# Kernel tuning notes

Measured on AMD Instinct MI355X. Metric: run time of the kernel, lower is better.

The kernel has to match this reference:

```python
import jax, jax.numpy as jnp
import numpy as np

N, B, D_IN, D_MID, D_OUT = 2048, 64, 768, 512, 128


def setup_inputs() -> dict:
    key = jax.random.key(0)
    ks = jax.random.split(key, 6)
    x = jax.random.normal(ks[0], (N, B, D_IN), dtype=jnp.float32)
    W1 = jax.random.normal(ks[1], (D_IN, D_MID), dtype=jnp.float32) * 0.02
    b1 = jax.random.normal(ks[2], (D_MID,), dtype=jnp.float32) * 0.02
    W2 = jax.random.normal(ks[3], (D_MID, D_OUT), dtype=jnp.float32) * 0.02
    b2 = jax.random.normal(ks[4], (D_OUT,), dtype=jnp.float32) * 0.02
    # per-sample segment lengths in [1, N//2] so segments are non-empty and in-range
    batch_list = jax.random.randint(ks[5], (B,), 1, N // 2, dtype=jnp.int32)
    return {"x": x, "W1": W1, "b1": b1, "W2": W2, "b2": b2,
            "batch_list": batch_list, "batch_size": B}


def reference(x, W1, b1, W2, b2, batch_list, batch_size):
    # x.reshape(-1, batch_size, 768).transpose(0, 1) -> (B, N, 768)
    xb = x.reshape(-1, batch_size, D_IN).transpose(1, 0, 2)
    h = jax.nn.relu(jnp.einsum('bnd,dm->bnm', xb, W1) + b1)
    x0 = jnp.einsum('bnm,mo->bno', h, W2) + b2  # (B, N, D_OUT)

    n = x0.shape[1]
    # torch code: batch_list.insert(0, 0); segment i = rows [L[i], L[i]+L[i+1]) of x_0[i]
    # i.e. start_i = (0 if i == 0 else batch_list[i-1]), len_i = batch_list[i]
    starts = jnp.concatenate([jnp.zeros((1,), jnp.int32), batch_list[:-1]])
    lens = batch_list
    j = jnp.arange(n, dtype=jnp.int32)  # (N,)
    mask = (j[None, :] >= starts[:, None]) & (j[None, :] < (starts + lens)[:, None])  # (B, N)
    neg = jnp.asarray(-jnp.inf, x0.dtype)
    x1 = jnp.where(mask[:, :, None], x0, neg).max(axis=1)  # (B, D_OUT)
    x1_probs = jnp.argmax(jax.nn.softmax(x1, axis=-1), axis=-1)
    return (x1, x1_probs)
```

## Files before the change

### kernel.cpp

```cpp
#include <hip/hip_runtime.h>
#include <math.h>

#define N_TOK 2048
#define BATCH 64
#define DIN   768
#define DMID  512
#define DOUT  128
#define TILE_N 64
#define KC    64
#define MC    128

__device__ __forceinline__ void atomicMaxFloat(float* addr, float val) {
    if (val >= 0.0f) atomicMax((int*)addr, __float_as_int(val));
    else             atomicMin((unsigned int*)addr, __float_as_uint(val));
}

__global__ void init_kernel(float* __restrict__ x1) {
    int i = blockIdx.x * blockDim.x + threadIdx.x;
    if (i < BATCH * DOUT) x1[i] = -INFINITY;
}

__global__ __launch_bounds__(256, 3) void fused_kernel(
    const float* __restrict__ x,
    const float* __restrict__ W1,
    const float* __restrict__ b1,
    const float* __restrict__ W2,
    const float* __restrict__ b2,
    const int*   __restrict__ batch_list,
    float* __restrict__ x1)
{
    const int b    = blockIdx.y;
    const int row0 = blockIdx.x * TILE_N;

    const int start = (b == 0) ? 0 : batch_list[b - 1];
    const int len   = batch_list[b];
    const int end   = start + len;
    if (row0 >= end || row0 + TILE_N <= start) return;

    __shared__ float xs[TILE_N][KC];
    __shared__ float hs[TILE_N][MC];

    const int tid = threadIdx.x;
    const int tr  = tid >> 5;
    const int tc  = tid & 31;

    float acc2[8][4];
    #pragma unroll
    for (int r = 0; r < 8; ++r)
        #pragma unroll
        for (int c = 0; c < 4; ++c) acc2[r][c] = 0.0f;

    for (int mc = 0; mc < DMID; mc += MC) {
        float acc1[8][4];
        #pragma unroll
        for (int r = 0; r < 8; ++r)
            #pragma unroll
            for (int c = 0; c < 4; ++c) acc1[r][c] = 0.0f;

        const float* W1c = W1 + mc + tc * 4;

        for (int kc = 0; kc < DIN; kc += KC) {
            __syncthreads();
            #pragma unroll
            for (int j = 0; j < 4; ++j) {
                const int i  = tid + j * 256;
                const int r  = i >> 4;
                const int kq = i & 15;
                *(float4*)&xs[r][kq * 4] =
                    *(const float4*)&x[((size_t)(row0 + r) * BATCH + b) * DIN + kc + kq * 4];
            }
            __syncthreads();

            #pragma unroll 4
            for (int k = 0; k < KC; ++k) {
                const float4 w = *(const float4*)&W1c[(size_t)(kc + k) * DMID];
                float xv[8];
                #pragma unroll
                for (int r = 0; r < 8; ++r) xv[r] = xs[tr * 8 + r][k];
                #pragma unroll
                for (int r = 0; r < 8; ++r) {
                    acc1[r][0] = fmaf(xv[r], w.x, acc1[r][0]);
                    acc1[r][1] = fmaf(xv[r], w.y, acc1[r][1]);
                    acc1[r][2] = fmaf(xv[r], w.z, acc1[r][2]);
                    acc1[r][3] = fmaf(xv[r], w.w, acc1[r][3]);
                }
            }
        }

        {
            const float4 bb = *(const float4*)&b1[mc + tc * 4];
            const float bv[4] = {bb.x, bb.y, bb.z, bb.w};
            #pragma unroll
            for (int r = 0; r < 8; ++r) {
                float4 hv;
                hv.x = fmaxf(acc1[r][0] + bv[0], 0.0f);
                hv.y = fmaxf(acc1[r][1] + bv[1], 0.0f);
                hv.z = fmaxf(acc1[r][2] + bv[2], 0.0f);
                hv.w = fmaxf(acc1[r][3] + bv[3], 0.0f);
                *(float4*)&hs[tr * 8 + r][tc * 4] = hv;
            }
        }
        __syncthreads();

        const float* W2c = W2 + (size_t)mc * DOUT + tc * 4;
        #pragma unroll 4
        for (int kk = 0; kk < MC; ++kk) {
            const float4 w = *(const float4*)&W2c[(size_t)kk * DOUT];
            float hv[8];
            #pragma unroll
            for (int r = 0; r < 8; ++r) hv[r] = hs[tr * 8 + r][kk];
            #pragma unroll
            for (int r = 0; r < 8; ++r) {
                acc2[r][0] = fmaf(hv[r], w.x, acc2[r][0]);
                acc2[r][1] = fmaf(hv[r], w.y, acc2[r][1]);
                acc2[r][2] = fmaf(hv[r], w.z, acc2[r][2]);
                acc2[r][3] = fmaf(hv[r], w.w, acc2[r][3]);
            }
        }
    }

    const float4 bb2 = *(const float4*)&b2[tc * 4];
    const float bv2[4] = {bb2.x, bb2.y, bb2.z, bb2.w};
    float cmax[4] = {-INFINITY, -INFINITY, -INFINITY, -INFINITY};
    #pragma unroll
    for (int r = 0; r < 8; ++r) {
        const int row = row0 + tr * 8 + r;
        const bool in = (row >= start) && (row < end);
        #pragma unroll
        for (int c = 0; c < 4; ++c) {
            const float v = acc2[r][c] + bv2[c];
            if (in) cmax[c] = fmaxf(cmax[c], v);
        }
    }

    float (*red)[DOUT] = (float(*)[DOUT])xs;
    #pragma unroll
    for (int c = 0; c < 4; ++c) red[tr][tc * 4 + c] = cmax[c];
    __syncthreads();

    if (tid < DOUT) {
        float m = red[0][tid];
        #pragma unroll
        for (int r = 1; r < 8; ++r) m = fmaxf(m, red[r][tid]);
        atomicMaxFloat(&x1[b * DOUT + tid], m);
    }
}

__global__ void argmax_kernel(const float* __restrict__ x1, float* __restrict__ probs) {
    int b = blockIdx.x * blockDim.x + threadIdx.x;
    if (b >= BATCH) return;
    const float* row = x1 + b * DOUT;
    float best = row[0];
    int bi = 0;
    for (int c = 1; c < DOUT; ++c) {
        float v = row[c];
        if (v > best) { best = v; bi = c; }
    }
    probs[b] = (float)bi;
}

extern "C" void kernel_launch(void* const* d_in, const int* in_sizes, int n_in,
                              void* d_out, int out_size, void* d_ws, size_t ws_size,
                              hipStream_t stream) {
    const float* x          = (const float*)d_in[0];
    const float* W1         = (const float*)d_in[1];
    const float* b1         = (const float*)d_in[2];
    const float* W2         = (const float*)d_in[3];
    const float* b2         = (const float*)d_in[4];
    const int*   batch_list = (const int*)d_in[5];

    float* x1    = (float*)d_out;
    float* probs = x1 + BATCH * DOUT;

    init_kernel<<<(BATCH * DOUT + 255) / 256, 256, 0, stream>>>(x1);

    dim3 grid(N_TOK / TILE_N, BATCH);
    fused_kernel<<<grid, 256, 0, stream>>>(x, W1, b1, W2, b2, batch_list, x1);

    argmax_kernel<<<1, 64, 0, stream>>>(x1, probs);
}
```

Before: 1.343 ms.

## Build compact work list of active tiles and run persistent grid with smaller tiles

A small prefix-sum kernel enumerates only the 32-row tiles that overlap each sample's segment and writes them to a work list. The fused MLP kernel then runs as a persistent grid of 1536 blocks that stride over this list, instead of launching a full 2D grid where most blocks exit early. The tile shrinks from 64 to 32 rows, and launch bounds allow 6 blocks per CU, trading per-block reuse of W1/W2 loads for finer-grained load balance and less wasted coverage. It adds an extra kernel launch and relies on the workspace buffer.

```diff
diff --git a/kernel.cpp b/kernel.cpp
--- a/kernel.cpp
+++ b/kernel.cpp
@@ -6,9 +6,11 @@
 #define DIN   768
 #define DMID  512
 #define DOUT  128
-#define TILE_N 64
+#define TILE  32
 #define KC    64
 #define MC    128
+#define GRID_B 1536
+#define MAX_ITEMS 4096
 
 __device__ __forceinline__ void atomicMaxFloat(float* addr, float val) {
     if (val >= 0.0f) atomicMax((int*)addr, __float_as_int(val));
@@ -20,129 +22,152 @@
     if (i < BATCH * DOUT) x1[i] = -INFINITY;
 }
 
-__global__ __launch_bounds__(256, 3) void fused_kernel(
+__global__ void build_kernel(const int* __restrict__ batch_list, int* __restrict__ ws) {
+    const int b     = threadIdx.x;
+    const int start = (b == 0) ? 0 : batch_list[b - 1];
+    const int len   = batch_list[b];
+    const int end   = start + len;
+    const int t0    = start >> 5;
+    const int t1    = (end - 1) >> 5;
+    const int n     = t1 - t0 + 1;
+
+    int incl = n;
+    #pragma unroll
+    for (int d = 1; d < 64; d <<= 1) {
+        int y = __shfl_up(incl, d);
+        if (b >= d) incl += y;
+    }
+    const int excl = incl - n;
+    if (b == 63) ws[0] = incl;
+    for (int t = 0; t < n; ++t)
+        ws[1 + excl + t] = (b << 16) | (t0 + t);
+}
+
+__global__ __launch_bounds__(256, 6) void fused_kernel(
     const float* __restrict__ x,
     const float* __restrict__ W1,
     const float* __restrict__ b1,
     const float* __restrict__ W2,
     const float* __restrict__ b2,
     const int*   __restrict__ batch_list,
+    const int*   __restrict__ ws,
     float* __restrict__ x1)
 {
-    const int b    = blockIdx.y;
-    const int row0 = blockIdx.x * TILE_N;
-
-    const int start = (b == 0) ? 0 : batch_list[b - 1];
-    const int len   = batch_list[b];
-    const int end   = start + len;
-    if (row0 >= end || row0 + TILE_N <= start) return;
-
-    __shared__ float xs[TILE_N][KC];
-    __shared__ float hs[TILE_N][MC];
+    __shared__ float xs[TILE][KC];
+    __shared__ float hs[TILE][MC];
 
     const int tid = threadIdx.x;
     const int tr  = tid >> 5;
     const int tc  = tid & 31;
 
-    float acc2[8][4];
-    #pragma unroll
-    for (int r = 0; r < 8; ++r)
+    int n_items = ws[0];
+    n_items = (n_items < 0) ? 0 : ((n_items > MAX_ITEMS) ? MAX_ITEMS : n_items);
+
+    for (int it = blockIdx.x; it < n_items; it += GRID_B) {
+        const int item = ws[1 + it];
+        const int b    = (item >> 16) & (BATCH - 1);
+        const int row0 = (item & (N_TOK / TILE - 1)) * TILE;
+        const int start = (b == 0) ? 0 : batch_list[b - 1];
+        const int end   = start + batch_list[b];
+
+        float acc2[4][4];
         #pragma unroll
-        for (int c = 0; c < 4; ++c) acc2[r][c] = 0.0f;
-
-    for (int mc = 0; mc < DMID; mc += MC) {
-        float acc1[8][4];
+        for (int r = 0; r < 4; ++r)
+            #pragma unroll
+            for (int c = 0; c < 4; ++c) acc2[r][c] = 0.0f;
+
+        for (int mc = 0; mc < DMID; mc += MC) {
+            float acc1[4][4];
+            #pragma unroll
+            for (int r = 0; r < 4; ++r)
+                #pragma unroll
+                for (int c = 0; c < 4; ++c) acc1[r][c] = 0.0f;
+
+            const float* W1c = W1 + mc + tc * 4;
+
+            for (int kc = 0; kc < DIN; kc += KC) {
+                __syncthreads();
+                #pragma unroll
+                for (int j = 0; j < 2; ++j) {
+                    const int i  = tid + j * 256;
+                    const int r  = i >> 4;
+                    const int kq = i & 15;
+                    *(float4*)&xs[r][kq * 4] =
+                        *(const float4*)&x[((size_t)(row0 + r) * BATCH + b) * DIN + kc + kq * 4];
+                }
+                __syncthreads();
+
+                #pragma unroll 4
+                for (int k = 0; k < KC; ++k) {
+                    const float4 w = *(const float4*)&W1c[(size_t)(kc + k) * DMID];
+                    float xv[4];
+                    #pragma unroll
+                    for (int r = 0; r < 4; ++r) xv[r] = xs[tr * 4 + r][k];
+                    #pragma unroll
+                    for (int r = 0; r < 4; ++r) {
+                        acc1[r][0] = fmaf(xv[r], w.x, acc1[r][0]);
+                        acc1[r][1] = fmaf(xv[r], w.y, acc1[r][1]);
+                        acc1[r][2] = fmaf(xv[r], w.z, acc1[r][2]);
+                        acc1[r][3] = fmaf(xv[r], w.w, acc1[r][3]);
+                    }
+                }
+            }
+
+            {
+                const float4 bb = *(const float4*)&b1[mc + tc * 4];
+                #pragma unroll
+                for (int r = 0; r < 4; ++r) {
+                    float4 hv;
+                    hv.x = fmaxf(acc1[r][0] + bb.x, 0.0f);
+                    hv.y = fmaxf(acc1[r][1] + bb.y, 0.0f);
+                    hv.z = fmaxf(acc1[r][2] + bb.z, 0.0f);
+                    hv.w = fmaxf(acc1[r][3] + bb.w, 0.0f);
+                    *(float4*)&hs[tr * 4 + r][tc * 4] = hv;
+                }
+            }
+            __syncthreads();
+
+            const float* W2c = W2 + (size_t)mc * DOUT + tc * 4;
+            #pragma unroll 4
+            for (int kk = 0; kk < MC; ++kk) {
+                const float4 w = *(const float4*)&W2c[(size_t)kk * DOUT];
+                float hv[4];
+                #pragma unroll
+                for (int r = 0; r < 4; ++r) hv[r] = hs[tr * 4 + r][kk];
+                #pragma unroll
+                for (int r = 0; r < 4; ++r) {
+                    acc2[r][0] = fmaf(hv[r], w.x, acc2[r][0]);
+                    acc2[r][1] = fmaf(hv[r], w.y, acc2[r][1]);
+                    acc2[r][2] = fmaf(hv[r], w.z, acc2[r][2]);
+                    acc2[r][3] = fmaf(hv[r], w.w, acc2[r][3]);
+                }
+            }
+        }
+
+        const float4 bb2 = *(const float4*)&b2[tc * 4];
+        float cmax[4] = {-INFINITY, -INFINITY, -INFINITY, -INFINITY};
         #pragma unroll
-        for (int r = 0; r < 8; ++r)
-            #pragma unroll
-            for (int c = 0; c < 4; ++c) acc1[r][c] = 0.0f;
-
-        const float* W1c = W1 + mc + tc * 4;
-
-        for (int kc = 0; kc < DIN; kc += KC) {
-            __syncthreads();
-            #pragma unroll
-            for (int j = 0; j < 4; ++j) {
-                const int i  = tid + j * 256;
-                const int r  = i >> 4;
-                const int kq = i & 15;
-                *(float4*)&xs[r][kq * 4] =
-                    *(const float4*)&x[((size_t)(row0 + r) * BATCH + b) * DIN + kc + kq * 4];
-            }
-            __syncthreads();
-
-            #pragma unroll 4
-            for (int k = 0; k < KC; ++k) {
-                const float4 w = *(const float4*)&W1c[(size_t)(kc + k) * DMID];
-                float xv[8];
-                #pragma unroll
-                for (int r = 0; r < 8; ++r) xv[r] = xs[tr * 8 + r][k];
-                #pragma unroll
-                for (int r = 0; r < 8; ++r) {
-                    acc1[r][0] = fmaf(xv[r], w.x, acc1[r][0]);
-                    acc1[r][1] = fmaf(xv[r], w.y, acc1[r][1]);
-                    acc1[r][2] = fmaf(xv[r], w.z, acc1[r][2]);
-                    acc1[r][3] = fmaf(xv[r], w.w, acc1[r][3]);
-                }
+        for (int r = 0; r < 4; ++r) {
+            const int row = row0 + tr * 4 + r;
+            const bool in = (row >= start) && (row < end);
+            #pragma unroll
+            for (int c = 0; c < 4; ++c) {
+                const float v = acc2[r][c] + ((const float*)&bb2)[c];
+                if (in) cmax[c] = fmaxf(cmax[c], v);
             }
         }
 
-        {
-            const float4 bb = *(const float4*)&b1[mc + tc * 4];
-            const float bv[4] = {bb.x, bb.y, bb.z, bb.w};
-            #pragma unroll
-            for (int r = 0; r < 8; ++r) {
-                float4 hv;
-                hv.x = fmaxf(acc1[r][0] + bv[0], 0.0f);
-                hv.y = fmaxf(acc1[r][1] + bv[1], 0.0f);
-                hv.z = fmaxf(acc1[r][2] + bv[2], 0.0f);
-                hv.w = fmaxf(acc1[r][3] + bv[3], 0.0f);
-                *(float4*)&hs[tr * 8 + r][tc * 4] = hv;
-            }
+        float (*red)[DOUT] = (float(*)[DOUT])xs;
+        #pragma unroll
+        for (int c = 0; c < 4; ++c) red[tr][tc * 4 + c] = cmax[c];
+        __syncthreads();
+
+        if (tid < DOUT) {
+            float m = red[0][tid];
+            #pragma unroll
+            for (int r = 1; r < 8; ++r) m = fmaxf(m, red[r][tid]);
+            atomicMaxFloat(&x1[b * DOUT + tid], m);
         }
-        __syncthreads();
-
-        const float* W2c = W2 + (size_t)mc * DOUT + tc * 4;
-        #pragma unroll 4
-        for (int kk = 0; kk < MC; ++kk) {
-            const float4 w = *(const float4*)&W2c[(size_t)kk * DOUT];
-            float hv[8];
-            #pragma unroll
-            for (int r = 0; r < 8; ++r) hv[r] = hs[tr * 8 + r][kk];
-            #pragma unroll
-            for (int r = 0; r < 8; ++r) {
-                acc2[r][0] = fmaf(hv[r], w.x, acc2[r][0]);
-                acc2[r][1] = fmaf(hv[r], w.y, acc2[r][1]);
-                acc2[r][2] = fmaf(hv[r], w.z, acc2[r][2]);
-                acc2[r][3] = fmaf(hv[r], w.w, acc2[r][3]);
-            }
-        }
-    }
-
-    const float4 bb2 = *(const float4*)&b2[tc * 4];
-    const float bv2[4] = {bb2.x, bb2.y, bb2.z, bb2.w};
-    float cmax[4] = {-INFINITY, -INFINITY, -INFINITY, -INFINITY};
-    #pragma unroll
-    for (int r = 0; r < 8; ++r) {
-        const int row = row0 + tr * 8 + r;
-        const bool in = (row >= start) && (row < end);
-        #pragma unroll
-        for (int c = 0; c < 4; ++c) {
-            const float v = acc2[r][c] + bv2[c];
-            if (in) cmax[c] = fmaxf(cmax[c], v);
-        }
-    }
-
-    float (*red)[DOUT] = (float(*)[DOUT])xs;
-    #pragma unroll
-    for (int c = 0; c < 4; ++c) red[tr][tc * 4 + c] = cmax[c];
-    __syncthreads();
-
-    if (tid < DOUT) {
-        float m = red[0][tid];
-        #pragma unroll
-        for (int r = 1; r < 8; ++r) m = fmaxf(m, red[r][tid]);
-        atomicMaxFloat(&x1[b * DOUT + tid], m);
     }
 }
 
@@ -171,11 +196,10 @@
 
     float* x1    = (float*)d_out;
     float* probs = x1 + BATCH * DOUT;
+    int*   ws    = (int*)d_ws;
 
     init_kernel<<<(BATCH * DOUT + 255) / 256, 256, 0, stream>>>(x1);
-
-    dim3 grid(N_TOK / TILE_N, BATCH);
-    fused_kernel<<<grid, 256, 0, stream>>>(x, W1, b1, W2, b2, batch_list, x1);
-
+    build_kernel<<<1, 64, 0, stream>>>(batch_list, ws);
+    fused_kernel<<<GRID_B, 256, 0, stream>>>(x, W1, b1, W2, b2, batch_list, ws, x1);
     argmax_kernel<<<1, 64, 0, stream>>>(x1, probs);
 }
```

Result: slower. 1.853 ms (+37.9%).
